# Kernel tuning notes

Hardware: AMD Instinct MI355X
Metric: run time of the kernel (lower is better)

The kernel has to match this reference:

```python
import jax, jax.numpy as jnp
import numpy as np

N_NODES = 50000
NEG_SLOPE_ATT = 0.2   # PyG GATConv default LeakyReLU slope for attention logits
NEG_SLOPE_ACT = 0.01  # nn.LeakyReLU default between layers


def _add_self_loops(src, dst, n):
    loop = jnp.arange(n, dtype=src.dtype)
    return jnp.concatenate([src, loop]), jnp.concatenate([dst, loop])


def gat_conv(x, W, a_src, a_dst, b, src, dst, n):
    # x: [N, Cin], W: [Cin, Cout], a_src/a_dst: [Cout], b: [Cout]
    h = x @ W                                   # [N, Cout]
    alpha_src = h @ a_src                       # [N]
    alpha_dst = h @ a_dst                       # [N]
    e = jax.nn.leaky_relu(alpha_src[src] + alpha_dst[dst], NEG_SLOPE_ATT)  # [E]
    # segment softmax over incoming edges of each dst node
    m = jax.ops.segment_max(e, dst, num_segments=n)      # [N]
    ex = jnp.exp(e - m[dst])                              # [E]
    s = jax.ops.segment_sum(ex, dst, num_segments=n)      # [N] (>0: self-loops)
    alpha = ex / s[dst]                                   # [E]
    out = jax.ops.segment_sum(h[src] * alpha[:, None], dst, num_segments=n)
    return out + b


def setup_inputs() -> dict:
    key = jax.random.key(0)
    ks = jax.random.split(key, 20)
    n, e = N_NODES, 800000
    cin, h1, h2, cout = 64, 128, 64, 32
    d = {
        "x": jax.random.normal(ks[0], (n, cin), jnp.float32),
        "edge_index": jax.random.randint(ks[1], (2, e), 0, n, jnp.int64),
    }
    dims = [(cin, h1), (h1, h2), (h2, h1), (h1, cout)]
    for i, (ci, co) in enumerate(dims, 1):
        g = 1.0 / np.sqrt(ci)
        d[f"W{i}"] = jax.random.normal(ks[2 + 4 * i], (ci, co), jnp.float32) * g
        d[f"a{i}s"] = jax.random.normal(ks[3 + 4 * i], (co,), jnp.float32) * 0.1
        d[f"a{i}d"] = jax.random.normal(ks[4 + 4 * i], (co,), jnp.float32) * 0.1
        d[f"b{i}"] = jnp.zeros((co,), jnp.float32)
    return d


def reference(x, edge_index, W1, a1s, a1d, b1, W2, a2s, a2d, b2,
              W3, a3s, a3d, b3, W4, a4s, a4d, b4):
    n = x.shape[0]
    src, dst = _add_self_loops(edge_index[0], edge_index[1], n)
    act = lambda t: jax.nn.leaky_relu(t, NEG_SLOPE_ACT)
    h = act(gat_conv(x, W1, a1s, a1d, b1, src, dst, n))
    # dropout is identity at inference
    h = act(gat_conv(h, W2, a2s, a2d, b2, src, dst, n))
    h = act(gat_conv(h, W3, a3s, a3d, b3, src, dst, n))
    return gat_conv(h, W4, a4s, a4d, b4, src, dst, n)
```

## Files before the change

### kernel.cpp

```cpp
#include <hip/hip_runtime.h>
#include <hip/hip_fp16.h>

#define NEG_ATT 0.2f


__global__ __launch_bounds__(256) void setup_k(int* cnt, int N, int NB,
                                               const float* __restrict__ W1, const float* __restrict__ a1s,
                                               const float* __restrict__ a1d, const float* __restrict__ W3,
                                               const float* __restrict__ a3s, const float* __restrict__ a3d,
                                               float* __restrict__ wa ,
                                               const float* __restrict__ x, __half* __restrict__ x16) {
    int b = blockIdx.x;
    if (b < NB) {
        int i = b * 256 + threadIdx.x;
        if (i < N) cnt[i] = 0;
    } else if (b == NB) {
        int t = threadIdx.x;
        int ci = t & 63;
        int which = t >> 6;
        const float* W = (which < 2) ? W1 : W3;
        const float* a = (which == 0) ? a1s : (which == 1) ? a1d : (which == 2) ? a3s : a3d;
        float s = 0.f;
        for (int co = 0; co < 128; ++co) s += W[ci * 128 + co] * a[co];
        wa[t] = s;
    } else {
        int i = (b - NB - 1) * 256 + threadIdx.x;
        if (i < (N * 64) / 4) {
            float4 v = *(const float4*)&x[(size_t)i * 4];
            __half2 p0 = __floats2half2_rn(v.x, v.y);
            __half2 p1 = __floats2half2_rn(v.z, v.w);
            uint2 pk = { *(unsigned*)&p0, *(unsigned*)&p1 };
            *(uint2*)&x16[(size_t)i * 4] = pk;
        }
    }
}


__global__ __launch_bounds__(256) void scatter_gemv_k(const int* __restrict__ src, const int* __restrict__ dst,
                                                      int* cnt, int* __restrict__ col,
                                                      int E, int step, int SB, int iters4,
                                                      const float* __restrict__ X,
                                                      const float* __restrict__ was, const float* __restrict__ wad,
                                                      float* __restrict__ as_, float* __restrict__ ad_, int N) {
    if (blockIdx.x < SB) {
        int part = blockIdx.x & 7;
        int lo = part * step, hi = lo + step;
        int tg = (blockIdx.x >> 3) * 256 + threadIdx.x;
        int stride = (SB >> 3) * 256;
        const int4* dst4 = (const int4*)dst;
        int E4 = E >> 2;
        for (int it = 0; it < iters4; ++it) {
            int i4 = tg + it * stride;
            if (i4 < E4) {
                int4 d4 = dst4[i4];
                int base = i4 << 2;
                if (d4.x >= lo && d4.x < hi) { int s = atomicAdd(&cnt[d4.x], 1); col[(d4.x << 6) + s] = src[base]; }
                if (d4.y >= lo && d4.y < hi) { int s = atomicAdd(&cnt[d4.y], 1); col[(d4.y << 6) + s] = src[base + 1]; }
                if (d4.z >= lo && d4.z < hi) { int s = atomicAdd(&cnt[d4.z], 1); col[(d4.z << 6) + s] = src[base + 2]; }
                if (d4.w >= lo && d4.w < hi) { int s = atomicAdd(&cnt[d4.w], 1); col[(d4.w << 6) + s] = src[base + 3]; }
            }
        }
    } else {
        int wid  = ((blockIdx.x - SB) * 256 + threadIdx.x) >> 6;
        int lane = threadIdx.x & 63;
        if (wid >= N) return;
        float xv = X[(size_t)wid * 64 + lane];
        float s1 = xv * was[lane];
        float s2 = xv * wad[lane];
        #pragma unroll
        for (int off = 32; off; off >>= 1) {
            s1 += __shfl_xor(s1, off);
            s2 += __shfl_xor(s2, off);
        }
        if (lane == 0) { as_[wid] = s1; ad_[wid] = s2; }
    }
}


__global__ __launch_bounds__(256) void gemm_wide_k(const float* __restrict__ X, const float* __restrict__ W,
                                                   const float* __restrict__ bias, float* __restrict__ H, int N) {
    __shared__ float Xs[128][68];
    __shared__ float Ws[64][128];
    int tid  = threadIdx.x;
    int row0 = blockIdx.x * 128;

    for (int i = tid; i < 2048; i += 256)
        *(float4*)&((float*)Ws)[i * 4] = *(const float4*)&W[i * 4];
    for (int i = tid; i < 2048; i += 256) {
        int r = i >> 4, k4 = i & 15;
        int gr = row0 + r;
        float4 v = {0.f, 0.f, 0.f, 0.f};
        if (gr < N) v = *(const float4*)&X[(size_t)gr * 64 + k4 * 4];
        *(float4*)&Xs[r][k4 * 4] = v;
    }
    __syncthreads();

    int ct = tid & 15;
    int rt = tid >> 4;
    float acc[8][8] = {};
    for (int k = 0; k < 64; k += 4) {
        float4 w0a = *(float4*)&Ws[k][ct * 8],     w0b = *(float4*)&Ws[k][ct * 8 + 4];
        float4 w1a = *(float4*)&Ws[k + 1][ct * 8], w1b = *(float4*)&Ws[k + 1][ct * 8 + 4];
        float4 w2a = *(float4*)&Ws[k + 2][ct * 8], w2b = *(float4*)&Ws[k + 2][ct * 8 + 4];
        float4 w3a = *(float4*)&Ws[k + 3][ct * 8], w3b = *(float4*)&Ws[k + 3][ct * 8 + 4];
        #pragma unroll
        for (int i = 0; i < 8; ++i) {
            float4 xv = *(float4*)&Xs[rt + 16 * i][k];
            acc[i][0] += xv.x * w0a.x + xv.y * w1a.x + xv.z * w2a.x + xv.w * w3a.x;
            acc[i][1] += xv.x * w0a.y + xv.y * w1a.y + xv.z * w2a.y + xv.w * w3a.y;
            acc[i][2] += xv.x * w0a.z + xv.y * w1a.z + xv.z * w2a.z + xv.w * w3a.z;
            acc[i][3] += xv.x * w0a.w + xv.y * w1a.w + xv.z * w2a.w + xv.w * w3a.w;
            acc[i][4] += xv.x * w0b.x + xv.y * w1b.x + xv.z * w2b.x + xv.w * w3b.x;
            acc[i][5] += xv.x * w0b.y + xv.y * w1b.y + xv.z * w2b.y + xv.w * w3b.y;
            acc[i][6] += xv.x * w0b.z + xv.y * w1b.z + xv.z * w2b.z + xv.w * w3b.z;
            acc[i][7] += xv.x * w0b.w + xv.y * w1b.w + xv.z * w2b.w + xv.w * w3b.w;
        }
    }

    float bv[8];
    #pragma unroll
    for (int j = 0; j < 8; ++j) bv[j] = bias[ct * 8 + j];

    #pragma unroll
    for (int i = 0; i < 8; ++i) {
        int gr = row0 + rt + 16 * i;
        if (gr < N) {
            float o[8];
            #pragma unroll
            for (int j = 0; j < 8; ++j) {
                float v = acc[i][j] + bv[j];
                o[j] = v > 0.f ? v : 0.01f * v;
            }
            *(float4*)&H[(size_t)gr * 128 + ct * 8]     = *(float4*)&o[0];
            *(float4*)&H[(size_t)gr * 128 + ct * 8 + 4] = *(float4*)&o[4];
        }
    }
}


template <int CIN, int COUT>
__global__ __launch_bounds__(256) void gemm_k(const float* __restrict__ X, const float* __restrict__ W,
                                              const float* __restrict__ a_s, const float* __restrict__ a_d,
                                              __half* __restrict__ Hh, float* __restrict__ as_,
                                              float* __restrict__ ad_, int N) {
    constexpr int RB  = (CIN == 128 && COUT == 64) ? 32 : 64;
    constexpr int NCT = COUT / 4;
    constexpr int NRT = 256 / NCT;
    constexpr int RT  = RB / NRT;
    constexpr int XP  = CIN + 4;
    __shared__ float Xs[RB][XP];
    __shared__ float Ws[CIN][COUT];
    int tid  = threadIdx.x;
    int row0 = blockIdx.x * RB;

    for (int i = tid; i < CIN * COUT / 4; i += 256)
        *(float4*)&((float*)Ws)[i * 4] = *(const float4*)&W[i * 4];
    for (int i = tid; i < RB * CIN / 4; i += 256) {
        int r = i / (CIN / 4), k4 = i % (CIN / 4);
        int gr = row0 + r;
        float4 v = {0.f, 0.f, 0.f, 0.f};
        if (gr < N) v = *(const float4*)&X[(size_t)gr * CIN + k4 * 4];
        *(float4*)&Xs[r][k4 * 4] = v;
    }
    __syncthreads();

    int ct = tid % NCT;
    int rt = tid / NCT;
    float acc[RT][4] = {};
    for (int k = 0; k < CIN; k += 4) {
        float4 w0 = *(float4*)&Ws[k][ct * 4];
        float4 w1 = *(float4*)&Ws[k + 1][ct * 4];
        float4 w2 = *(float4*)&Ws[k + 2][ct * 4];
        float4 w3 = *(float4*)&Ws[k + 3][ct * 4];
        #pragma unroll
        for (int i = 0; i < RT; ++i) {
            float4 xv = *(float4*)&Xs[rt + i * NRT][k];
            acc[i][0] += xv.x * w0.x + xv.y * w1.x + xv.z * w2.x + xv.w * w3.x;
            acc[i][1] += xv.x * w0.y + xv.y * w1.y + xv.z * w2.y + xv.w * w3.y;
            acc[i][2] += xv.x * w0.z + xv.y * w1.z + xv.z * w2.z + xv.w * w3.z;
            acc[i][3] += xv.x * w0.w + xv.y * w1.w + xv.z * w2.w + xv.w * w3.w;
        }
    }

    float asv[4], adv[4];
    #pragma unroll
    for (int j = 0; j < 4; ++j) { asv[j] = a_s[ct * 4 + j]; adv[j] = a_d[ct * 4 + j]; }

    #pragma unroll
    for (int i = 0; i < RT; ++i) {
        int gr = row0 + rt + i * NRT;
        float s1 = acc[i][0] * asv[0] + acc[i][1] * asv[1] + acc[i][2] * asv[2] + acc[i][3] * asv[3];
        float s2 = acc[i][0] * adv[0] + acc[i][1] * adv[1] + acc[i][2] * adv[2] + acc[i][3] * adv[3];
        #pragma unroll
        for (int off = 1; off < NCT; off <<= 1) {
            s1 += __shfl_xor(s1, off);
            s2 += __shfl_xor(s2, off);
        }
        if (gr < N) {
            __half2 p0 = __floats2half2_rn(acc[i][0], acc[i][1]);
            __half2 p1 = __floats2half2_rn(acc[i][2], acc[i][3]);
            uint2 pk = { *(unsigned*)&p0, *(unsigned*)&p1 };
            *(uint2*)&Hh[(size_t)gr * COUT + ct * 4] = pk;
            if (ct == 0) { as_[gr] = s1; ad_[gr] = s2; }
        }
    }
}


template <int C, int MODE>
__global__ __launch_bounds__(256) void agg_k(const __half* __restrict__ Hg, const float* __restrict__ as_,
                                             const float* __restrict__ ad_, const int* __restrict__ deg,
                                             const int* __restrict__ col, const float* __restrict__ bias,
                                             const float* __restrict__ was, const float* __restrict__ wad,
                                             float* __restrict__ outf, __half* __restrict__ outh,
                                             float* __restrict__ oas, float* __restrict__ oad, int N) {
    __shared__ int2 sw[4][64];
    int wid  = (blockIdx.x * 256 + threadIdx.x) >> 6;
    int lane = threadIdx.x & 63;
    int wvi  = threadIdx.x >> 6;
    if (wid >= N) return;
    float adi = ad_[wid];
    int dg = deg[wid];
    float a0 = 0.f, a1 = 0.f, a2 = 0.f, a3 = 0.f;
    const int sub = lane >> 5;
    const int c32 = lane & 31;

    int s_l = 0; float w_l = 0.f;
    if (lane < dg) {
        s_l = col[(wid << 6) + lane];
        float e = as_[s_l] + adi;
        e = e > 0.f ? e : NEG_ATT * e;
        w_l = __expf(e);
    }
    sw[wvi][lane] = make_int2(s_l, __float_as_int(w_l));

    float es = as_[wid] + adi;
    es = es > 0.f ? es : NEG_ATT * es;
    float ws = __expf(es);
    float denom = w_l + ((lane == 0) ? ws : 0.f);
    if (C == 64) {
        a0 += ws * __half2float(Hg[((size_t)wid << 6) | lane]);
    } else {
        if (!sub) a0 += ws * __half2float(Hg[((size_t)wid << 5) | c32]);
    }

    auto g16 = [&](int j) {
        float hv[16], wv[16];
        #pragma unroll
        for (int u = 0; u < 16; ++u) {
            int2 p = sw[wvi][j + u];
            wv[u] = __int_as_float(p.y);
            hv[u] = __half2float(Hg[((size_t)p.x << 6) | lane]);
        }
        #pragma unroll
        for (int u = 0; u < 16; u += 4) {
            a0 += wv[u] * hv[u]; a1 += wv[u + 1] * hv[u + 1];
            a2 += wv[u + 2] * hv[u + 2]; a3 += wv[u + 3] * hv[u + 3];
        }
    };
    auto g8 = [&](int j) {
        float hv[8], wv[8];
        #pragma unroll
        for (int u = 0; u < 8; ++u) {
            int2 p = sw[wvi][j + u];
            wv[u] = __int_as_float(p.y);
            hv[u] = __half2float(Hg[((size_t)p.x << 6) | lane]);
        }
        #pragma unroll
        for (int u = 0; u < 8; u += 4) {
            a0 += wv[u] * hv[u]; a1 += wv[u + 1] * hv[u + 1];
            a2 += wv[u + 2] * hv[u + 2]; a3 += wv[u + 3] * hv[u + 3];
        }
    };
    auto g4 = [&](int j) {
        float hv[4], wv[4];
        #pragma unroll
        for (int u = 0; u < 4; ++u) {
            int2 p = sw[wvi][j + u];
            wv[u] = __int_as_float(p.y);
            hv[u] = __half2float(Hg[((size_t)p.x << 6) | lane]);
        }
        a0 += wv[0] * hv[0]; a1 += wv[1] * hv[1];
        a2 += wv[2] * hv[2]; a3 += wv[3] * hv[3];
    };
    auto g16_32 = [&](int j) {
        float hv[8], wv[8];
        #pragma unroll
        for (int u = 0; u < 8; ++u) {
            int2 p = sw[wvi][j + 2 * u + sub];
            wv[u] = __int_as_float(p.y);
            hv[u] = __half2float(Hg[((size_t)p.x << 5) | c32]);
        }
        #pragma unroll
        for (int u = 0; u < 8; u += 4) {
            a0 += wv[u] * hv[u]; a1 += wv[u + 1] * hv[u + 1];
            a2 += wv[u + 2] * hv[u + 2]; a3 += wv[u + 3] * hv[u + 3];
        }
    };
    auto g8_32 = [&](int j) {
        float hv[4], wv[4];
        #pragma unroll
        for (int u = 0; u < 4; ++u) {
            int2 p = sw[wvi][j + 2 * u + sub];
            wv[u] = __int_as_float(p.y);
            hv[u] = __half2float(Hg[((size_t)p.x << 5) | c32]);
        }
        a0 += wv[0] * hv[0]; a1 += wv[1] * hv[1];
        a2 += wv[2] * hv[2]; a3 += wv[3] * hv[3];
    };

    int j = 0;
    if (C == 64) {
        for (; j + 16 <= dg; j += 16) g16(j);
        int rem = dg - j;
        if (rem > 8) g16(j);
        else if (rem > 4) g8(j);
        else if (rem > 0) g4(j);
    } else {
        for (; j + 16 <= dg; j += 16) g16_32(j);
        int rem = dg - j;
        if (rem > 8) g16_32(j);
        else if (rem > 0) g8_32(j);
    }

    float acc = (a0 + a1) + (a2 + a3);
    #pragma unroll
    for (int off = 32; off; off >>= 1) denom += __shfl_xor(denom, off);
    if (C == 32) acc += __shfl_xor(acc, 32);

    float inv = 1.f / denom;
    float v = acc * inv;
    if (MODE == 1) {
        v += bias[lane];
        v = v > 0.f ? v : 0.01f * v;
        outh[((size_t)wid << 6) | lane] = __float2half(v);
        float s1 = v * was[lane];
        float s2 = v * wad[lane];
        #pragma unroll
        for (int off = 32; off; off >>= 1) {
            s1 += __shfl_xor(s1, off);
            s2 += __shfl_xor(s2, off);
        }
        if (lane == 0) { oas[wid] = s1; oad[wid] = s2; }
    } else if (MODE == 2) {
        if (lane < 32) outf[((size_t)wid << 5) | c32] = v + bias[c32];
    } else {
        outf[((size_t)wid << 6) | lane] = v;
    }
}


extern "C" void kernel_launch(void* const* d_in, const int* in_sizes, int n_in,
                              void* d_out, int out_size, void* d_ws, size_t ws_size,
                              hipStream_t stream) {
    const float* x  = (const float*)d_in[0];
    const int* ei   = (const int*)d_in[1];
    const float* W1 = (const float*)d_in[2];
    const float* a1s = (const float*)d_in[3];
    const float* a1d = (const float*)d_in[4];
    const float* b1  = (const float*)d_in[5];
    const float* W2 = (const float*)d_in[6];
    const float* a2s = (const float*)d_in[7];
    const float* a2d = (const float*)d_in[8];
    const float* b2  = (const float*)d_in[9];
    const float* W3 = (const float*)d_in[10];
    const float* a3s = (const float*)d_in[11];
    const float* a3d = (const float*)d_in[12];
    const float* b3  = (const float*)d_in[13];
    const float* W4 = (const float*)d_in[14];
    const float* a4s = (const float*)d_in[15];
    const float* a4d = (const float*)d_in[16];
    const float* b4  = (const float*)d_in[17];

    const int N = in_sizes[0] / 64;
    const int E = in_sizes[1] / 2;
    const int* src = ei;
    const int* dst = ei + E;

    float* bufT = (float*)d_ws;
    float* bufH = bufT + (size_t)N * 64;
    float* asA  = bufH + (size_t)N * 128;
    float* adA  = asA + N;
    float* asB  = adA + N;
    float* adB  = asB + N;
    float* wa   = adB + N;
    int* cnt    = (int*)(wa + 256);
    int* col    = cnt + N;
    __half* x16 = (__half*)(col + (size_t)N * 64);
    __half* g1  = x16 + (size_t)N * 64;
    __half* g2  = g1 + (size_t)N * 64;

    const int NB = (N + 255) / 256;
    const int XB = (N * 64 / 4 + 255) / 256;
    const int STEP = (N + 7) / 8;
    const int SB = 2048;
    const int ITERS4 = ((E >> 2) + (SB / 8) * 256 - 1) / ((SB / 8) * 256);
    const int NWAVE = (N * 64 + 255) / 256;

    setup_k<<<NB + 1 + XB, 256, 0, stream>>>(cnt, N, NB, W1, a1s, a1d, W3, a3s, a3d, wa, x, x16);
    float* wa1s = wa, *wa1d = wa + 64, *wa3s = wa + 128, *wa3d = wa + 192;

    scatter_gemv_k<<<SB + NWAVE, 256, 0, stream>>>(src, dst, cnt, col, E, STEP, SB, ITERS4,
                                                   x, wa1s, wa1d, asA, adA, N);

    agg_k<64, 0><<<NWAVE, 256, 0, stream>>>(x16, asA, adA, cnt, col, nullptr, nullptr, nullptr,
                                            bufT, nullptr, nullptr, nullptr, N);
    gemm_wide_k<<<(N + 127) / 128, 256, 0, stream>>>(bufT, W1, b1, bufH, N);

    gemm_k<128, 64><<<(N + 31) / 32, 256, 0, stream>>>(bufH, W2, a2s, a2d, g1, asB, adB, N);
    agg_k<64, 1><<<NWAVE, 256, 0, stream>>>(g1, asB, adB, cnt, col, b2, wa3s, wa3d,
                                            nullptr, g2, asA, adA, N);

    agg_k<64, 0><<<NWAVE, 256, 0, stream>>>(g2, asA, adA, cnt, col, nullptr, nullptr, nullptr,
                                            bufT, nullptr, nullptr, nullptr, N);
    gemm_wide_k<<<(N + 127) / 128, 256, 0, stream>>>(bufT, W3, b3, bufH, N);

    gemm_k<128, 32><<<(N + 63) / 64, 256, 0, stream>>>(bufH, W4, a4s, a4d, g1, asB, adB, N);
    agg_k<32, 2><<<NWAVE, 256, 0, stream>>>(g1, asB, adB, cnt, col, b4, nullptr, nullptr,
                                            (float*)d_out, nullptr, nullptr, nullptr, N);
}
```

Baseline: 246.2 us.

## Vectorize half2 gathers in aggregation and store aggregated features as fp16

The aggregation kernel now has each lane load a half2, so one wave handles two edges (or four for C=32) per load, and the partial sums are combined with cross-lane shuffles. MODE 0 writes its aggregated output as fp16 into a new buffer, and the wide GEMM reads and converts that fp16 input, which halves that intermediate traffic. The CSR scatter also reads src as int4 with a fixed-unroll loop and gains a scalar tail for edge counts not divisible by four. The fp16 intermediate adds rounding error, and the scatter loop caps iterations at 4, which silently drops edges if iters4 exceeds 4.

```diff
diff --git a/kernel.cpp b/kernel.cpp
--- a/kernel.cpp
+++ b/kernel.cpp
@@ -48,17 +48,24 @@
         int tg = (blockIdx.x >> 3) * 256 + threadIdx.x;
         int stride = (SB >> 3) * 256;
         const int4* dst4 = (const int4*)dst;
+        const int4* src4 = (const int4*)src;
         int E4 = E >> 2;
-        for (int it = 0; it < iters4; ++it) {
+        #pragma unroll
+        for (int it = 0; it < 4; ++it) {
+            if (it >= iters4) break;
             int i4 = tg + it * stride;
             if (i4 < E4) {
                 int4 d4 = dst4[i4];
-                int base = i4 << 2;
-                if (d4.x >= lo && d4.x < hi) { int s = atomicAdd(&cnt[d4.x], 1); col[(d4.x << 6) + s] = src[base]; }
-                if (d4.y >= lo && d4.y < hi) { int s = atomicAdd(&cnt[d4.y], 1); col[(d4.y << 6) + s] = src[base + 1]; }
-                if (d4.z >= lo && d4.z < hi) { int s = atomicAdd(&cnt[d4.z], 1); col[(d4.z << 6) + s] = src[base + 2]; }
-                if (d4.w >= lo && d4.w < hi) { int s = atomicAdd(&cnt[d4.w], 1); col[(d4.w << 6) + s] = src[base + 3]; }
+                int4 s4 = src4[i4];
+                if (d4.x >= lo && d4.x < hi) { int s = atomicAdd(&cnt[d4.x], 1); col[(d4.x << 6) + s] = s4.x; }
+                if (d4.y >= lo && d4.y < hi) { int s = atomicAdd(&cnt[d4.y], 1); col[(d4.y << 6) + s] = s4.y; }
+                if (d4.z >= lo && d4.z < hi) { int s = atomicAdd(&cnt[d4.z], 1); col[(d4.z << 6) + s] = s4.z; }
+                if (d4.w >= lo && d4.w < hi) { int s = atomicAdd(&cnt[d4.w], 1); col[(d4.w << 6) + s] = s4.w; }
             }
+        }
+        for (int i = (E & ~3) + tg; i < E; i += stride) {
+            int d = dst[i];
+            if (d >= lo && d < hi) { int s = atomicAdd(&cnt[d], 1); col[(d << 6) + s] = src[i]; }
         }
     } else {
         int wid  = ((blockIdx.x - SB) * 256 + threadIdx.x) >> 6;
@@ -77,7 +84,7 @@
 }
 
 
-__global__ __launch_bounds__(256) void gemm_wide_k(const float* __restrict__ X, const float* __restrict__ W,
+__global__ __launch_bounds__(256) void gemm_wide_k(const __half* __restrict__ X16, const float* __restrict__ W,
                                                    const float* __restrict__ bias, float* __restrict__ H, int N) {
     __shared__ float Xs[128][68];
     __shared__ float Ws[64][128];
@@ -90,7 +97,12 @@
         int r = i >> 4, k4 = i & 15;
         int gr = row0 + r;
         float4 v = {0.f, 0.f, 0.f, 0.f};
-        if (gr < N) v = *(const float4*)&X[(size_t)gr * 64 + k4 * 4];
+        if (gr < N) {
+            uint2 pk = *(const uint2*)&X16[(size_t)gr * 64 + k4 * 4];
+            float2 f0 = __half22float2(*(__half2*)&pk.x);
+            float2 f1 = __half22float2(*(__half2*)&pk.y);
+            v = make_float4(f0.x, f0.y, f1.x, f1.y);
+        }
         *(float4*)&Xs[r][k4 * 4] = v;
     }
     __syncthreads();
@@ -221,9 +233,9 @@
     if (wid >= N) return;
     float adi = ad_[wid];
     int dg = deg[wid];
-    float a0 = 0.f, a1 = 0.f, a2 = 0.f, a3 = 0.f;
-    const int sub = lane >> 5;
-    const int c32 = lane & 31;
+    float a0 = 0.f, a1 = 0.f, b0 = 0.f, b1 = 0.f;
+    const int sub  = lane >> 5, c32 = lane & 31;
+    const int quad = lane >> 4, c16 = lane & 15;
 
     int s_l = 0; float w_l = 0.f;
     if (lane < dg) {
@@ -239,113 +251,102 @@
     float ws = __expf(es);
     float denom = w_l + ((lane == 0) ? ws : 0.f);
     if (C == 64) {
-        a0 += ws * __half2float(Hg[((size_t)wid << 6) | lane]);
+        if (!sub) {
+            float2 f = __half22float2(*(const __half2*)&Hg[((size_t)wid << 6) + 2 * c32]);
+            a0 += ws * f.x; a1 += ws * f.y;
+        }
     } else {
-        if (!sub) a0 += ws * __half2float(Hg[((size_t)wid << 5) | c32]);
-    }
-
-    auto g16 = [&](int j) {
-        float hv[16], wv[16];
-        #pragma unroll
-        for (int u = 0; u < 16; ++u) {
-            int2 p = sw[wvi][j + u];
-            wv[u] = __int_as_float(p.y);
-            hv[u] = __half2float(Hg[((size_t)p.x << 6) | lane]);
-        }
-        #pragma unroll
-        for (int u = 0; u < 16; u += 4) {
-            a0 += wv[u] * hv[u]; a1 += wv[u + 1] * hv[u + 1];
-            a2 += wv[u + 2] * hv[u + 2]; a3 += wv[u + 3] * hv[u + 3];
-        }
-    };
-    auto g8 = [&](int j) {
-        float hv[8], wv[8];
-        #pragma unroll
-        for (int u = 0; u < 8; ++u) {
-            int2 p = sw[wvi][j + u];
-            wv[u] = __int_as_float(p.y);
-            hv[u] = __half2float(Hg[((size_t)p.x << 6) | lane]);
-        }
-        #pragma unroll
-        for (int u = 0; u < 8; u += 4) {
-            a0 += wv[u] * hv[u]; a1 += wv[u + 1] * hv[u + 1];
-            a2 += wv[u + 2] * hv[u + 2]; a3 += wv[u + 3] * hv[u + 3];
-        }
-    };
-    auto g4 = [&](int j) {
-        float hv[4], wv[4];
-        #pragma unroll
-        for (int u = 0; u < 4; ++u) {
-            int2 p = sw[wvi][j + u];
-            wv[u] = __int_as_float(p.y);
-            hv[u] = __half2float(Hg[((size_t)p.x << 6) | lane]);
-        }
-        a0 += wv[0] * hv[0]; a1 += wv[1] * hv[1];
-        a2 += wv[2] * hv[2]; a3 += wv[3] * hv[3];
-    };
-    auto g16_32 = [&](int j) {
-        float hv[8], wv[8];
-        #pragma unroll
-        for (int u = 0; u < 8; ++u) {
+        if (!quad) {
+            float2 f = __half22float2(*(const __half2*)&Hg[((size_t)wid << 5) + 2 * c16]);
+            a0 += ws * f.x; a1 += ws * f.y;
+        }
+    }
+
+    auto g64 = [&](int j, auto NEhalf) {
+        constexpr int M = decltype(NEhalf)::value;
+        float2 hv[M]; float wv[M];
+        #pragma unroll
+        for (int u = 0; u < M; ++u) {
             int2 p = sw[wvi][j + 2 * u + sub];
             wv[u] = __int_as_float(p.y);
-            hv[u] = __half2float(Hg[((size_t)p.x << 5) | c32]);
-        }
-        #pragma unroll
-        for (int u = 0; u < 8; u += 4) {
-            a0 += wv[u] * hv[u]; a1 += wv[u + 1] * hv[u + 1];
-            a2 += wv[u + 2] * hv[u + 2]; a3 += wv[u + 3] * hv[u + 3];
+            hv[u] = __half22float2(*(const __half2*)&Hg[((size_t)p.x << 6) + 2 * c32]);
+        }
+        #pragma unroll
+        for (int u = 0; u < M; ++u) {
+            if (u & 1) { b0 += wv[u] * hv[u].x; b1 += wv[u] * hv[u].y; }
+            else       { a0 += wv[u] * hv[u].x; a1 += wv[u] * hv[u].y; }
         }
     };
-    auto g8_32 = [&](int j) {
-        float hv[4], wv[4];
-        #pragma unroll
-        for (int u = 0; u < 4; ++u) {
-            int2 p = sw[wvi][j + 2 * u + sub];
+    auto g32 = [&](int j, auto NEq) {
+        constexpr int M = decltype(NEq)::value;
+        float2 hv[M]; float wv[M];
+        #pragma unroll
+        for (int u = 0; u < M; ++u) {
+            int2 p = sw[wvi][j + 4 * u + quad];
             wv[u] = __int_as_float(p.y);
-            hv[u] = __half2float(Hg[((size_t)p.x << 5) | c32]);
-        }
-        a0 += wv[0] * hv[0]; a1 += wv[1] * hv[1];
-        a2 += wv[2] * hv[2]; a3 += wv[3] * hv[3];
+            hv[u] = __half22float2(*(const __half2*)&Hg[((size_t)p.x << 5) + 2 * c16]);
+        }
+        #pragma unroll
+        for (int u = 0; u < M; ++u) {
+            if (u & 1) { b0 += wv[u] * hv[u].x; b1 += wv[u] * hv[u].y; }
+            else       { a0 += wv[u] * hv[u].x; a1 += wv[u] * hv[u].y; }
+        }
     };
 
     int j = 0;
     if (C == 64) {
-        for (; j + 16 <= dg; j += 16) g16(j);
+        for (; j + 16 <= dg; j += 16) g64(j, std::integral_constant<int, 8>{});
         int rem = dg - j;
-        if (rem > 8) g16(j);
-        else if (rem > 4) g8(j);
-        else if (rem > 0) g4(j);
+        if (rem > 8) g64(j, std::integral_constant<int, 8>{});
+        else if (rem > 4) g64(j, std::integral_constant<int, 4>{});
+        else if (rem > 0) g64(j, std::integral_constant<int, 2>{});
     } else {
-        for (; j + 16 <= dg; j += 16) g16_32(j);
+        for (; j + 16 <= dg; j += 16) g32(j, std::integral_constant<int, 4>{});
         int rem = dg - j;
-        if (rem > 8) g16_32(j);
-        else if (rem > 0) g8_32(j);
-    }
-
-    float acc = (a0 + a1) + (a2 + a3);
+        if (rem > 8) g32(j, std::integral_constant<int, 4>{});
+        else if (rem > 4) g32(j, std::integral_constant<int, 2>{});
+        else if (rem > 0) g32(j, std::integral_constant<int, 1>{});
+    }
+
+    float f0 = a0 + b0, f1 = a1 + b1;
+    if (C == 32) { f0 += __shfl_xor(f0, 16); f1 += __shfl_xor(f1, 16); }
+    f0 += __shfl_xor(f0, 32); f1 += __shfl_xor(f1, 32);
     #pragma unroll
     for (int off = 32; off; off >>= 1) denom += __shfl_xor(denom, off);
-    if (C == 32) acc += __shfl_xor(acc, 32);
 
     float inv = 1.f / denom;
-    float v = acc * inv;
-    if (MODE == 1) {
-        v += bias[lane];
-        v = v > 0.f ? v : 0.01f * v;
-        outh[((size_t)wid << 6) | lane] = __float2half(v);
-        float s1 = v * was[lane];
-        float s2 = v * wad[lane];
-        #pragma unroll
-        for (int off = 32; off; off >>= 1) {
+    float v0 = f0 * inv, v1 = f1 * inv;
+
+    if (MODE == 0) {
+        if (!sub) {
+            __half2 p = __floats2half2_rn(v0, v1);
+            *(__half2*)&outh[((size_t)wid << 6) + 2 * c32] = p;
+        }
+    } else if (MODE == 1) {
+        float2 bb = *(const float2*)&bias[2 * c32];
+        v0 += bb.x; v1 += bb.y;
+        v0 = v0 > 0.f ? v0 : 0.01f * v0;
+        v1 = v1 > 0.f ? v1 : 0.01f * v1;
+        if (!sub) {
+            __half2 p = __floats2half2_rn(v0, v1);
+            *(__half2*)&outh[((size_t)wid << 6) + 2 * c32] = p;
+        }
+        float2 wsv = *(const float2*)&was[2 * c32];
+        float2 wdv = *(const float2*)&wad[2 * c32];
+        float s1 = v0 * wsv.x + v1 * wsv.y;
+        float s2 = v0 * wdv.x + v1 * wdv.y;
+        #pragma unroll
+        for (int off = 16; off; off >>= 1) {
             s1 += __shfl_xor(s1, off);
             s2 += __shfl_xor(s2, off);
         }
         if (lane == 0) { oas[wid] = s1; oad[wid] = s2; }
-    } else if (MODE == 2) {
-        if (lane < 32) outf[((size_t)wid << 5) | c32] = v + bias[c32];
     } else {
-        outf[((size_t)wid << 6) | lane] = v;
+        if (!quad) {
+            float2 bb = *(const float2*)&bias[2 * c16];
+            float2 o = {v0 + bb.x, v1 + bb.y};
+            *(float2*)&outf[((size_t)wid << 5) + 2 * c16] = o;
+        }
     }
 }
 
@@ -377,8 +378,7 @@
     const int* src = ei;
     const int* dst = ei + E;
 
-    float* bufT = (float*)d_ws;
-    float* bufH = bufT + (size_t)N * 64;
+    float* bufH = (float*)d_ws;
     float* asA  = bufH + (size_t)N * 128;
     float* adA  = asA + N;
     float* asB  = adA + N;
@@ -389,6 +389,7 @@
     __half* x16 = (__half*)(col + (size_t)N * 64);
     __half* g1  = x16 + (size_t)N * 64;
     __half* g2  = g1 + (size_t)N * 64;
+    __half* g3  = g2 + (size_t)N * 64;
 
     const int NB = (N + 255) / 256;
     const int XB = (N * 64 / 4 + 255) / 256;
@@ -404,16 +405,16 @@
                                                    x, wa1s, wa1d, asA, adA, N);
 
     agg_k<64, 0><<<NWAVE, 256, 0, stream>>>(x16, asA, adA, cnt, col, nullptr, nullptr, nullptr,
-                                            bufT, nullptr, nullptr, nullptr, N);
-    gemm_wide_k<<<(N + 127) / 128, 256, 0, stream>>>(bufT, W1, b1, bufH, N);
+                                            nullptr, g3, nullptr, nullptr, N);
+    gemm_wide_k<<<(N + 127) / 128, 256, 0, stream>>>(g3, W1, b1, bufH, N);
 
     gemm_k<128, 64><<<(N + 31) / 32, 256, 0, stream>>>(bufH, W2, a2s, a2d, g1, asB, adB, N);
     agg_k<64, 1><<<NWAVE, 256, 0, stream>>>(g1, asB, adB, cnt, col, b2, wa3s, wa3d,
                                             nullptr, g2, asA, adA, N);
 
     agg_k<64, 0><<<NWAVE, 256, 0, stream>>>(g2, asA, adA, cnt, col, nullptr, nullptr, nullptr,
-                                            bufT, nullptr, nullptr, nullptr, N);
-    gemm_wide_k<<<(N + 127) / 128, 256, 0, stream>>>(bufT, W3, b3, bufH, N);
+                                            nullptr, g3, nullptr, nullptr, N);
+    gemm_wide_k<<<(N + 127) / 128, 256, 0, stream>>>(g3, W3, b3, bufH, N);
 
     gemm_k<128, 32><<<(N + 63) / 64, 256, 0, stream>>>(bufH, W4, a4s, a4d, g1, asB, adB, N);
     agg_k<32, 2><<<NWAVE, 256, 0, stream>>>(g1, asB, adB, cnt, col, b4, nullptr, nullptr,
```

After: 243.7 us. Within noise of the previous version (-1.0%).
